# Performance work log

Hardware: AMD Instinct MI355X
Metric: run time of the kernel (lower is better)

Reference implementation:

```python
import jax, jax.numpy as jnp
import numpy as np

N = 65536       # n_nodes
E = 1048576     # n_edges (avg degree 16)
IDX = 256       # index_size
DIN = 512       # gcn_input_size
DH = 512        # gcn_hidden_size
DOUT = 128      # gcn_output_size
S = 256         # sample_size


def gcn_conv(h, W, b, src, dst, n):
    # PyG GCNConv: linear, add self-loops, symmetric deg^-1/2 normalization, scatter-add.
    h = h @ W
    loop = jnp.arange(n)
    s = jnp.concatenate([src, loop])
    d = jnp.concatenate([dst, loop])
    deg = jax.ops.segment_sum(jnp.ones(s.shape[0], h.dtype), d, num_segments=n)
    inv_sqrt = jax.lax.rsqrt(deg)  # deg >= 1 due to self-loops
    norm = inv_sqrt[s] * inv_sqrt[d]
    out = jax.ops.segment_sum(h[s] * norm[:, None], d, num_segments=n)
    return out + b


def _lin_init(k, fan_in, shape):
    bound = 1.0 / np.sqrt(fan_in)
    return jax.random.uniform(k, shape, jnp.float32, -bound, bound)


def setup_inputs() -> dict:
    key = jax.random.key(0)
    ks = jax.random.split(key, 14)
    x = jax.random.normal(ks[0], (N, IDX + 768), jnp.float32)
    edge_index = jax.random.randint(ks[1], (2, E), 0, N, dtype=jnp.int64)
    return {
        "x": x,
        "W_t1": _lin_init(ks[2], IDX, (IDX, DIN)),
        "b_t1": _lin_init(ks[3], IDX, (DIN,)),
        "W_t2": _lin_init(ks[4], 768, (768, DIN)),
        "b_t2": _lin_init(ks[5], 768, (DIN,)),
        "W1": _lin_init(ks[6], DIN, (DIN, DH)),
        "b1": _lin_init(ks[7], DIN, (DH,)),
        "W2": _lin_init(ks[8], DH, (DH, DOUT)),
        "b2": _lin_init(ks[9], DH, (DOUT,)),
        "matrix": jax.random.normal(ks[10], (DOUT, DOUT), jnp.float32),
        "lin_w": _lin_init(ks[11], 1, (2,)),   # nn.Linear(1, 2) weight, squeezed
        "lin_b": _lin_init(ks[12], 1, (2,)),
        "edge_index": edge_index,
    }


def reference(x, W_t1, b_t1, W_t2, b_t2, W1, b1, W2, b2, matrix, lin_w, lin_b, edge_index):
    src, dst = edge_index[0], edge_index[1]
    # dual-input linear fusion
    h = x[:, :IDX] @ W_t1 + b_t1 + x[:, IDX:] @ W_t2 + b_t2
    h = gcn_conv(h, W1, b1, src, dst, N)
    h = jax.nn.relu(h)  # dropout is identity in eval mode
    h = gcn_conv(h, W2, b2, src, dst, N)
    # per-sample bilinear score, batched over chunks
    e = h.reshape(N // S, S, DOUT)
    scores = jnp.einsum('bid,de,bje->bij', e, matrix, e)  # [B, S, S]
    out = scores[..., None] * lin_w + lin_b               # Linear(1, 2)
    return out.reshape(-1, 2)
```

## Files before the change

### kernel.cpp

```cpp
#include <hip/hip_runtime.h>
#include <stdint.h>

#define NN 65536

typedef __attribute__((ext_vector_type(8))) short bf16x8;
typedef __attribute__((ext_vector_type(4))) float f32x4;

__device__ __forceinline__ unsigned short f2bf(float f) {
    unsigned u = __float_as_uint(f);
    u += 0x7fffu + ((u >> 16) & 1u);
    return (unsigned short)(u >> 16);
}
__device__ __forceinline__ float bf2f(unsigned short h) { return __uint_as_float(((unsigned)h) << 16); }
__device__ __forceinline__ float blo(unsigned u) { return __uint_as_float(u << 16); }
__device__ __forceinline__ float bhi(unsigned u) { return __uint_as_float(u & 0xffff0000u); }
__device__ __forceinline__ unsigned pack2(float a, float b) {
    return ((unsigned)f2bf(b) << 16) | (unsigned)f2bf(a);
}

__device__ __forceinline__ void gl_lds16(const void* g, void* l) {
    __builtin_amdgcn_global_load_lds((const __attribute__((address_space(1))) void*)g,
                                     (__attribute__((address_space(3))) void*)l, 16, 0, 0);
}

__global__ void prep_pack(const float* Wt1, const float* Wt2, const float* W1,
                          const float* W2, const float* Mtx,
                          unsigned short* Wcat, unsigned short* W1T,
                          unsigned short* W2T, unsigned short* MTh, unsigned short* MTl) {
    int i = blockIdx.x * 256 + threadIdx.x;
    if (i < 524288) {
        int k = i >> 9, j = i & 511;
        float v = (k < 256) ? Wt1[k * 512 + j] : Wt2[(k - 256) * 512 + j];
        Wcat[i] = f2bf(v);
    } else if (i < 786432) {
        int t = i - 524288; int n = t >> 9, j = t & 511;
        W1T[t] = f2bf(W1[j * 512 + n]);
    } else if (i < 851968) {
        int t = i - 786432; int n = t >> 9, j = t & 511;
        W2T[t] = f2bf(W2[j * 128 + n]);
    } else if (i < 868352) {
        int t = i - 851968; int d = t >> 7, e = t & 127;
        float m = Mtx[e * 128 + d];
        unsigned short h = f2bf(m);
        MTh[t] = h; MTl[t] = f2bf(m - bf2f(h));
    }
}

__global__ void cbias_k(const float* bt1, const float* bt2, const float* W1, float* c) {
    int n = blockIdx.x * 256 + threadIdx.x;
    float acc = 0.f;
    for (int j = 0; j < 512; j++) acc += (bt1[j] + bt2[j]) * W1[j * 512 + n];
    c[n] = acc;
}

__global__ void count_k(const int* dst, int* cnt, int E) {
    int e = blockIdx.x * 256 + threadIdx.x;
    if (e < E) atomicAdd(&cnt[dst[e]], 1);
}
__global__ void red_k(const int* cnt, int* bsum) {
    __shared__ int sm[256];
    int tid = threadIdx.x;
    sm[tid] = cnt[blockIdx.x * 256 + tid];
    __syncthreads();
    for (int s = 128; s > 0; s >>= 1) {
        if (tid < s) sm[tid] += sm[tid + s];
        __syncthreads();
    }
    if (tid == 0) bsum[blockIdx.x] = sm[0];
}
__global__ void scanb_k(const int* bsum, int* boff) {
    __shared__ int sm[256];
    int tid = threadIdx.x;
    int v0 = bsum[tid];
    sm[tid] = v0;
    __syncthreads();
    for (int s = 1; s < 256; s <<= 1) {
        int t = sm[tid];
        if (tid >= s) t += sm[tid - s];
        __syncthreads();
        sm[tid] = t;
        __syncthreads();
    }
    boff[tid] = sm[tid] - v0;
}
__global__ void scanf_k(const int* cnt, const int* boff, int* rowptr, int* cursor, float* invs) {
    __shared__ int sm[256];
    int tid = threadIdx.x;
    int i = blockIdx.x * 256 + tid;
    int v = cnt[i];
    sm[tid] = v;
    __syncthreads();
    for (int s = 1; s < 256; s <<= 1) {
        int t = sm[tid];
        if (tid >= s) t += sm[tid - s];
        __syncthreads();
        sm[tid] = t;
        __syncthreads();
    }
    int incl = sm[tid];
    int base = boff[blockIdx.x];
    int excl = base + incl - v;
    rowptr[i] = excl;
    cursor[i] = excl;
    invs[i] = rsqrtf((float)(v + 1));
    if (i == NN - 1) rowptr[NN] = base + incl;
}
__global__ void fill_k(const int* src, const int* dst, int* cursor, int* colv, int E) {
    int e = blockIdx.x * 256 + threadIdx.x;
    if (e < E) {
        int d = dst[e];
        int p = atomicAdd(&cursor[d], 1);
        colv[p] = src[e];
    }
}

__global__ __launch_bounds__(256, 2) void gemm_bt(const unsigned short* A, const unsigned short* BT,
                                                  unsigned short* C, const float* bias,
                                                  int M, int N, int K) {
    __shared__ __align__(16) unsigned short sA[128 * 32];
    __shared__ __align__(16) unsigned short sB[128 * 32];
    int tid = threadIdx.x, wave = tid >> 6, lane = tid & 63;
    int bm = blockIdx.y * 128, bn = blockIdx.x * 128;
    int wm = (wave >> 1) * 64, wn = (wave & 1) * 64;
    f32x4 acc[4][4];
#pragma unroll
    for (int i = 0; i < 4; i++)
#pragma unroll
        for (int j = 0; j < 4; j++) acc[i][j] = (f32x4){0.f, 0.f, 0.f, 0.f};
    int sr = wave * 32 + (lane >> 2);
    int sc = (lane & 3) * 8;
    const int fr = lane & 15;
    const int fk = (lane >> 4) * 8;
    for (int k0 = 0; k0 < K; k0 += 32) {
        const unsigned short* ga = A + (size_t)(bm + sr) * K + k0 + sc;
        gl_lds16(ga, &sA[sr * 32 + sc]);
        gl_lds16(ga + (size_t)16 * K, &sA[(sr + 16) * 32 + sc]);
        const unsigned short* gb = BT + (size_t)(bn + sr) * K + k0 + sc;
        gl_lds16(gb, &sB[sr * 32 + sc]);
        gl_lds16(gb + (size_t)16 * K, &sB[(sr + 16) * 32 + sc]);
        __syncthreads();
        bf16x8 af[4], bfr[4];
#pragma unroll
        for (int i = 0; i < 4; i++) af[i] = *(const bf16x8*)&sA[(wm + i * 16 + fr) * 32 + fk];
#pragma unroll
        for (int j = 0; j < 4; j++) bfr[j] = *(const bf16x8*)&sB[(wn + j * 16 + fr) * 32 + fk];
#pragma unroll
        for (int i = 0; i < 4; i++)
#pragma unroll
            for (int j = 0; j < 4; j++)
                acc[i][j] = __builtin_amdgcn_mfma_f32_16x16x32_bf16(af[i], bfr[j], acc[i][j], 0, 0, 0);
        __syncthreads();
    }
    int rq = (lane >> 4) * 4;
#pragma unroll
    for (int i = 0; i < 4; i++)
#pragma unroll
        for (int j = 0; j < 4; j++) {
            int col = bn + wn + j * 16 + fr;
            float bb = bias ? bias[col] : 0.f;
#pragma unroll
            for (int r = 0; r < 4; r++) {
                int row = bm + wm + i * 16 + rq + r;
                C[(size_t)row * N + col] = f2bf(acc[i][j][r] + bb);
            }
        }
}

__global__ __launch_bounds__(256, 2) void gemm_f32a(const float* A, const unsigned short* BT,
                                                    unsigned short* C, const float* bias,
                                                    int M, int N, int K) {
    __shared__ __align__(16) unsigned short sA[128 * 32];
    __shared__ __align__(16) unsigned short sB[128 * 32];
    int tid = threadIdx.x, wave = tid >> 6, lane = tid & 63;
    int bm = blockIdx.y * 128, bn = blockIdx.x * 128;
    int wm = (wave >> 1) * 64, wn = (wave & 1) * 64;
    f32x4 acc[4][4];
#pragma unroll
    for (int i = 0; i < 4; i++)
#pragma unroll
        for (int j = 0; j < 4; j++) acc[i][j] = (f32x4){0.f, 0.f, 0.f, 0.f};
    int sr = wave * 32 + (lane >> 2);
    int sc = (lane & 3) * 8;
    const int fr = lane & 15;
    const int fk = (lane >> 4) * 8;
    for (int k0 = 0; k0 < K; k0 += 32) {
#pragma unroll
        for (int i = 0; i < 4; i++) {
            int idx = tid + 256 * i;
            int row = idx >> 3, cg = idx & 7;
            float4 v = *(const float4*)&A[(size_t)(bm + row) * K + k0 + cg * 4];
            ushort4 pk;
            pk.x = f2bf(v.x); pk.y = f2bf(v.y); pk.z = f2bf(v.z); pk.w = f2bf(v.w);
            *(ushort4*)&sA[row * 32 + cg * 4] = pk;
        }
        const unsigned short* gb = BT + (size_t)(bn + sr) * K + k0 + sc;
        gl_lds16(gb, &sB[sr * 32 + sc]);
        gl_lds16(gb + (size_t)16 * K, &sB[(sr + 16) * 32 + sc]);
        __syncthreads();
        bf16x8 af[4], bfr[4];
#pragma unroll
        for (int i = 0; i < 4; i++) af[i] = *(const bf16x8*)&sA[(wm + i * 16 + fr) * 32 + fk];
#pragma unroll
        for (int j = 0; j < 4; j++) bfr[j] = *(const bf16x8*)&sB[(wn + j * 16 + fr) * 32 + fk];
#pragma unroll
        for (int i = 0; i < 4; i++)
#pragma unroll
            for (int j = 0; j < 4; j++)
                acc[i][j] = __builtin_amdgcn_mfma_f32_16x16x32_bf16(af[i], bfr[j], acc[i][j], 0, 0, 0);
        __syncthreads();
    }
    int rq = (lane >> 4) * 4;
#pragma unroll
    for (int i = 0; i < 4; i++)
#pragma unroll
        for (int j = 0; j < 4; j++) {
            int col = bn + wn + j * 16 + fr;
            float bb = bias ? bias[col] : 0.f;
#pragma unroll
            for (int r = 0; r < 4; r++) {
                int row = bm + wm + i * 16 + rq + r;
                C[(size_t)row * N + col] = f2bf(acc[i][j][r] + bb);
            }
        }
}

__global__ __launch_bounds__(256, 2) void gemm_T(const unsigned short* h2h, const unsigned short* h2l,
                                                 const unsigned short* MTh, const unsigned short* MTl,
                                                 unsigned short* Th, unsigned short* Tl) {
    __shared__ __align__(16) unsigned short sA[128 * 32];
    __shared__ __align__(16) unsigned short sB[128 * 32];
    int tid = threadIdx.x, wave = tid >> 6, lane = tid & 63;
    int bm = blockIdx.x * 128;
    int wm = (wave >> 1) * 64, wn = (wave & 1) * 64;
    f32x4 acc[4][4];
#pragma unroll
    for (int i = 0; i < 4; i++)
#pragma unroll
        for (int j = 0; j < 4; j++) acc[i][j] = (f32x4){0.f, 0.f, 0.f, 0.f};
    int sr = wave * 32 + (lane >> 2);
    int sc = (lane & 3) * 8;
    const int fr = lane & 15;
    const int fk = (lane >> 4) * 8;
    const unsigned short* APs[3] = {h2h, h2h, h2l};
    const unsigned short* BPs[3] = {MTh, MTl, MTh};
    for (int it = 0; it < 12; it++) {
        int ph = it >> 2, k0 = (it & 3) * 32;
        const unsigned short* ga = APs[ph] + (size_t)(bm + sr) * 128 + k0 + sc;
        gl_lds16(ga, &sA[sr * 32 + sc]);
        gl_lds16(ga + 16 * 128, &sA[(sr + 16) * 32 + sc]);
        const unsigned short* gb = BPs[ph] + (size_t)sr * 128 + k0 + sc;
        gl_lds16(gb, &sB[sr * 32 + sc]);
        gl_lds16(gb + 16 * 128, &sB[(sr + 16) * 32 + sc]);
        __syncthreads();
        bf16x8 af[4], bfr[4];
#pragma unroll
        for (int i = 0; i < 4; i++) af[i] = *(const bf16x8*)&sA[(wm + i * 16 + fr) * 32 + fk];
#pragma unroll
        for (int j = 0; j < 4; j++) bfr[j] = *(const bf16x8*)&sB[(wn + j * 16 + fr) * 32 + fk];
#pragma unroll
        for (int i = 0; i < 4; i++)
#pragma unroll
            for (int j = 0; j < 4; j++)
                acc[i][j] = __builtin_amdgcn_mfma_f32_16x16x32_bf16(af[i], bfr[j], acc[i][j], 0, 0, 0);
        __syncthreads();
    }
    int rq = (lane >> 4) * 4;
#pragma unroll
    for (int i = 0; i < 4; i++)
#pragma unroll
        for (int j = 0; j < 4; j++) {
            int col = wn + j * 16 + fr;
#pragma unroll
            for (int r = 0; r < 4; r++) {
                int row = bm + wm + i * 16 + rq + r;
                float v = acc[i][j][r];
                unsigned short h = f2bf(v);
                Th[(size_t)row * 128 + col] = h;
                Tl[(size_t)row * 128 + col] = f2bf(v - bf2f(h));
            }
        }
}

__global__ __launch_bounds__(256) void agg512(const unsigned short* t, const int* rowptr,
                                              const int* colv, const float* invs,
                                              const float* bias, unsigned short* outp) {
    int wave = threadIdx.x >> 6, lane = threadIdx.x & 63;
    int node = blockIdx.x * 4 + wave;
    int d0 = lane * 8;
    float acc[8] = {0.f, 0.f, 0.f, 0.f, 0.f, 0.f, 0.f, 0.f};
    int r0 = rowptr[node], r1 = rowptr[node + 1];
    for (int e = r0; e < r1; e++) {
        int s = colv[e];
        float ws = invs[s];
        uint4 v = *(const uint4*)&t[(size_t)s * 512 + d0];
        acc[0] += ws * blo(v.x); acc[1] += ws * bhi(v.x);
        acc[2] += ws * blo(v.y); acc[3] += ws * bhi(v.y);
        acc[4] += ws * blo(v.z); acc[5] += ws * bhi(v.z);
        acc[6] += ws * blo(v.w); acc[7] += ws * bhi(v.w);
    }
    float wd = invs[node], wdd = wd * wd;
    uint4 sv = *(const uint4*)&t[(size_t)node * 512 + d0];
    float sf[8] = {blo(sv.x), bhi(sv.x), blo(sv.y), bhi(sv.y), blo(sv.z), bhi(sv.z), blo(sv.w), bhi(sv.w)};
    float o[8];
#pragma unroll
    for (int k = 0; k < 8; k++) {
        float v = acc[k] * wd + sf[k] * wdd + bias[d0 + k];
        o[k] = v > 0.f ? v : 0.f;
    }
    uint4 pv;
    pv.x = pack2(o[0], o[1]); pv.y = pack2(o[2], o[3]);
    pv.z = pack2(o[4], o[5]); pv.w = pack2(o[6], o[7]);
    *(uint4*)&outp[(size_t)node * 512 + d0] = pv;
}

__global__ __launch_bounds__(256) void agg128(const unsigned short* u, const int* rowptr,
                                              const int* colv, const float* invs,
                                              const float* bias, unsigned short* h2h, unsigned short* h2l) {
    int wave = threadIdx.x >> 6, lane = threadIdx.x & 63;
    int node = blockIdx.x * 4 + wave;
    int q = lane >> 4, ql = lane & 15;
    int d0 = ql * 8;
    float acc[8] = {0.f, 0.f, 0.f, 0.f, 0.f, 0.f, 0.f, 0.f};
    int r0 = rowptr[node], r1 = rowptr[node + 1];
    for (int e = r0 + q; e < r1; e += 4) {
        int s = colv[e];
        float ws = invs[s];
        uint4 v = *(const uint4*)&u[(size_t)s * 128 + d0];
        acc[0] += ws * blo(v.x); acc[1] += ws * bhi(v.x);
        acc[2] += ws * blo(v.y); acc[3] += ws * bhi(v.y);
        acc[4] += ws * blo(v.z); acc[5] += ws * bhi(v.z);
        acc[6] += ws * blo(v.w); acc[7] += ws * bhi(v.w);
    }
#pragma unroll
    for (int k = 0; k < 8; k++) {
        acc[k] += __shfl_xor(acc[k], 16);
        acc[k] += __shfl_xor(acc[k], 32);
    }
    float wd = invs[node], wdd = wd * wd;
    uint4 sv = *(const uint4*)&u[(size_t)node * 128 + d0];
    float sf[8] = {blo(sv.x), bhi(sv.x), blo(sv.y), bhi(sv.y), blo(sv.z), bhi(sv.z), blo(sv.w), bhi(sv.w)};
    unsigned short hh[8], hl[8];
#pragma unroll
    for (int k = 0; k < 8; k++) {
        float v = acc[k] * wd + sf[k] * wdd + bias[d0 + k];
        hh[k] = f2bf(v);
        hl[k] = f2bf(v - bf2f(hh[k]));
    }
    if (q == 0) {
        uint4 ph, pl;
        ph.x = ((unsigned)hh[1] << 16) | hh[0]; ph.y = ((unsigned)hh[3] << 16) | hh[2];
        ph.z = ((unsigned)hh[5] << 16) | hh[4]; ph.w = ((unsigned)hh[7] << 16) | hh[6];
        pl.x = ((unsigned)hl[1] << 16) | hl[0]; pl.y = ((unsigned)hl[3] << 16) | hl[2];
        pl.z = ((unsigned)hl[5] << 16) | hl[4]; pl.w = ((unsigned)hl[7] << 16) | hl[6];
        *(uint4*)&h2h[(size_t)node * 128 + d0] = ph;
        *(uint4*)&h2l[(size_t)node * 128 + d0] = pl;
    }
}

__global__ __launch_bounds__(256, 2) void bilinear_k(const unsigned short* Th, const unsigned short* Tl,
                                                     const unsigned short* Eh, const float* lin_w,
                                                     const float* lin_b, float* outp) {
    int tid = threadIdx.x, wave = tid >> 6, lane = tid & 63;
    int b = blockIdx.x >> 1, half = blockIdx.x & 1;
    int fr = lane & 15, q = lane >> 4;
    int irow0 = b * 256 + half * 128 + wave * 32;
    bf16x8 Ah[2][4], Al[2][4];
#pragma unroll
    for (int it = 0; it < 2; it++)
#pragma unroll
        for (int kk = 0; kk < 4; kk++) {
            size_t off = (size_t)(irow0 + it * 16 + fr) * 128 + kk * 32 + q * 8;
            Ah[it][kk] = *(const bf16x8*)&Th[off];
            Al[it][kk] = *(const bf16x8*)&Tl[off];
        }
    float w0 = lin_w[0], w1 = lin_w[1], c0 = lin_b[0], c1 = lin_b[1];
    for (int jt = 0; jt < 16; jt++) {
        bf16x8 Bf[4];
#pragma unroll
        for (int kk = 0; kk < 4; kk++)
            Bf[kk] = *(const bf16x8*)&Eh[(size_t)(b * 256 + jt * 16 + fr) * 128 + kk * 32 + q * 8];
#pragma unroll
        for (int it = 0; it < 2; it++) {
            f32x4 acc = (f32x4){0.f, 0.f, 0.f, 0.f};
#pragma unroll
            for (int kk = 0; kk < 4; kk++) {
                acc = __builtin_amdgcn_mfma_f32_16x16x32_bf16(Ah[it][kk], Bf[kk], acc, 0, 0, 0);
                acc = __builtin_amdgcn_mfma_f32_16x16x32_bf16(Al[it][kk], Bf[kk], acc, 0, 0, 0);
            }
#pragma unroll
            for (int r = 0; r < 4; r++) {
                int iloc = half * 128 + wave * 32 + it * 16 + q * 4 + r;
                int jloc = jt * 16 + fr;
                size_t o = ((size_t)b * 65536 + (size_t)iloc * 256 + jloc) * 2;
                float s = acc[r];
                float2 ov;
                ov.x = fmaf(s, w0, c0);
                ov.y = fmaf(s, w1, c1);
                *(float2*)&outp[o] = ov;
            }
        }
    }
}

extern "C" void kernel_launch(void* const* d_in, const int* in_sizes, int n_in,
                              void* d_out, int out_size, void* d_ws, size_t ws_size,
                              hipStream_t stream) {
    const float* x   = (const float*)d_in[0];
    const float* Wt1 = (const float*)d_in[1];
    const float* bt1 = (const float*)d_in[2];
    const float* Wt2 = (const float*)d_in[3];
    const float* bt2 = (const float*)d_in[4];
    const float* W1  = (const float*)d_in[5];
    const float* b1  = (const float*)d_in[6];
    const float* W2  = (const float*)d_in[7];
    const float* b2  = (const float*)d_in[8];
    const float* Mtx = (const float*)d_in[9];
    const float* lw  = (const float*)d_in[10];
    const float* lb  = (const float*)d_in[11];
    const int*   ei  = (const int*)d_in[12];
    int E = in_sizes[12] / 2;
    const int* srcp = ei;
    const int* dstp = ei + E;

    unsigned char* p = (unsigned char*)d_ws;
    size_t off = 0;
    auto alloc = [&](size_t bytes) -> void* {
        void* r = p + off;
        off = (off + bytes + 255) & ~(size_t)255;
        return r;
    };
    int*   cnt    = (int*)alloc((size_t)NN * 4);
    int*   rowptr = (int*)alloc(((size_t)NN + 1) * 4);
    int*   cursor = (int*)alloc((size_t)NN * 4);
    float* invs   = (float*)alloc((size_t)NN * 4);
    int*   bsum   = (int*)alloc(256 * 4);
    int*   boff   = (int*)alloc(256 * 4);
    int*   colv   = (int*)alloc((size_t)E * 4);
    unsigned short* Wcat   = (unsigned short*)alloc(524288 * 2);
    unsigned short* W1T    = (unsigned short*)alloc(262144 * 2);
    unsigned short* W2T    = (unsigned short*)alloc(65536 * 2);
    unsigned short* MTh    = (unsigned short*)alloc(16384 * 2);
    unsigned short* MTl    = (unsigned short*)alloc(16384 * 2);
    float*          cbias  = (float*)alloc(512 * 4);
    unsigned short* WcombT = (unsigned short*)alloc(524288 * 2);
    unsigned short* t1     = (unsigned short*)alloc((size_t)NN * 512 * 2);
    unsigned short* h1     = (unsigned short*)alloc((size_t)NN * 512 * 2);
    unsigned short* uu     = (unsigned short*)alloc((size_t)NN * 128 * 2);
    unsigned short* Th  = t1;
    unsigned short* Tl  = t1 + (size_t)NN * 128;
    unsigned short* h2h = h1;
    unsigned short* h2l = h1 + (size_t)NN * 128;

    hipMemsetAsync(cnt, 0, (size_t)NN * 4, stream);
    prep_pack<<<3392, 256, 0, stream>>>(Wt1, Wt2, W1, W2, Mtx, Wcat, W1T, W2T, MTh, MTl);
    cbias_k<<<2, 256, 0, stream>>>(bt1, bt2, W1, cbias);
    count_k<<<(E + 255) / 256, 256, 0, stream>>>(dstp, cnt, E);
    red_k<<<256, 256, 0, stream>>>(cnt, bsum);
    scanb_k<<<1, 256, 0, stream>>>(bsum, boff);
    scanf_k<<<256, 256, 0, stream>>>(cnt, boff, rowptr, cursor, invs);
    fill_k<<<(E + 255) / 256, 256, 0, stream>>>(srcp, dstp, cursor, colv, E);
    gemm_bt<<<dim3(8, 4), 256, 0, stream>>>(W1T, Wcat, WcombT, nullptr, 512, 1024, 512);
    gemm_f32a<<<dim3(4, 512), 256, 0, stream>>>(x, WcombT, t1, cbias, NN, 512, 1024);
    agg512<<<NN / 4, 256, 0, stream>>>(t1, rowptr, colv, invs, b1, h1);
    gemm_bt<<<dim3(1, 512), 256, 0, stream>>>(h1, W2T, uu, nullptr, NN, 128, 512);
    agg128<<<NN / 4, 256, 0, stream>>>(uu, rowptr, colv, invs, b2, h2h, h2l);
    gemm_T<<<512, 256, 0, stream>>>(h2h, h2l, MTh, MTl, Th, Tl);
    bilinear_k<<<512, 256, 0, stream>>>(Th, Tl, h2h, lw, lb, (float*)d_out);
}
```

Baseline: 952.2 us.

## Double-buffer f32 GEMM, remap blocks by XCD, unroll aggregation, split bias reduction

```diff
diff --git a/kernel.cpp b/kernel.cpp
--- a/kernel.cpp
+++ b/kernel.cpp
@@ -47,10 +47,21 @@
 }
 
 __global__ void cbias_k(const float* bt1, const float* bt2, const float* W1, float* c) {
-    int n = blockIdx.x * 256 + threadIdx.x;
+    __shared__ float sm[256];
+    int t = threadIdx.x;
+    int n = blockIdx.x * 32 + (t & 31);
+    int jp = t >> 5;
     float acc = 0.f;
-    for (int j = 0; j < 512; j++) acc += (bt1[j] + bt2[j]) * W1[j * 512 + n];
-    c[n] = acc;
+    for (int j = jp * 64; j < jp * 64 + 64; j++)
+        acc += (bt1[j] + bt2[j]) * W1[j * 512 + n];
+    sm[t] = acc;
+    __syncthreads();
+    if (t < 32) {
+        float a = 0.f;
+#pragma unroll
+        for (int p = 0; p < 8; p++) a += sm[p * 32 + t];
+        c[blockIdx.x * 32 + t] = a;
+    }
 }
 
 __global__ void count_k(const int* dst, int* cnt, int E) {
@@ -167,12 +178,14 @@
 }
 
 __global__ __launch_bounds__(256, 2) void gemm_f32a(const float* A, const unsigned short* BT,
-                                                    unsigned short* C, const float* bias,
-                                                    int M, int N, int K) {
-    __shared__ __align__(16) unsigned short sA[128 * 32];
-    __shared__ __align__(16) unsigned short sB[128 * 32];
+                                                    unsigned short* C, const float* bias) {
+    const int K = 1024, N = 512;
+    __shared__ __align__(16) unsigned short sA[2][128 * 32];
+    __shared__ __align__(16) unsigned short sB[2][128 * 32];
     int tid = threadIdx.x, wave = tid >> 6, lane = tid & 63;
-    int bm = blockIdx.y * 128, bn = blockIdx.x * 128;
+    int b = blockIdx.x;
+    int xcd = b & 7, jn = (b >> 3) & 3, tt = b >> 5;
+    int bm = (tt * 8 + xcd) * 128, bn = jn * 128;
     int wm = (wave >> 1) * 64, wn = (wave & 1) * 64;
     f32x4 acc[4][4];
 #pragma unroll
@@ -183,25 +196,44 @@
     int sc = (lane & 3) * 8;
     const int fr = lane & 15;
     const int fk = (lane >> 4) * 8;
-    for (int k0 = 0; k0 < K; k0 += 32) {
+    int ar = tid >> 3, ac = (tid & 7) * 4;
+    const float* Abase = A + (size_t)(bm + ar) * K + ac;
+    const unsigned short* Bbase = BT + (size_t)(bn + sr) * K + sc;
+    float4 ra[4];
+    auto loadA = [&](int k0) {
+#pragma unroll
+        for (int i = 0; i < 4; i++)
+            ra[i] = *(const float4*)(Abase + (size_t)(32 * i) * K + k0);
+    };
+    auto stageA = [&](int buf) {
 #pragma unroll
         for (int i = 0; i < 4; i++) {
-            int idx = tid + 256 * i;
-            int row = idx >> 3, cg = idx & 7;
-            float4 v = *(const float4*)&A[(size_t)(bm + row) * K + k0 + cg * 4];
             ushort4 pk;
-            pk.x = f2bf(v.x); pk.y = f2bf(v.y); pk.z = f2bf(v.z); pk.w = f2bf(v.w);
-            *(ushort4*)&sA[row * 32 + cg * 4] = pk;
-        }
-        const unsigned short* gb = BT + (size_t)(bn + sr) * K + k0 + sc;
-        gl_lds16(gb, &sB[sr * 32 + sc]);
-        gl_lds16(gb + (size_t)16 * K, &sB[(sr + 16) * 32 + sc]);
-        __syncthreads();
+            pk.x = f2bf(ra[i].x); pk.y = f2bf(ra[i].y); pk.z = f2bf(ra[i].z); pk.w = f2bf(ra[i].w);
+            *(ushort4*)&sA[buf][(ar + 32 * i) * 32 + ac] = pk;
+        }
+    };
+    auto stageB = [&](int buf, int k0) {
+        gl_lds16(Bbase + k0, &sB[buf][sr * 32 + sc]);
+        gl_lds16(Bbase + (size_t)16 * K + k0, &sB[buf][(sr + 16) * 32 + sc]);
+    };
+    loadA(0);
+    stageB(0, 0);
+    stageA(0);
+    loadA(32);
+    __syncthreads();
+    for (int k = 0; k < 32; k++) {
+        int cur = k & 1, nxt = cur ^ 1;
+        if (k < 31) {
+            stageB(nxt, (k + 1) * 32);
+            stageA(nxt);
+        }
+        if (k < 30) loadA((k + 2) * 32);
         bf16x8 af[4], bfr[4];
 #pragma unroll
-        for (int i = 0; i < 4; i++) af[i] = *(const bf16x8*)&sA[(wm + i * 16 + fr) * 32 + fk];
-#pragma unroll
-        for (int j = 0; j < 4; j++) bfr[j] = *(const bf16x8*)&sB[(wn + j * 16 + fr) * 32 + fk];
+        for (int i = 0; i < 4; i++) af[i] = *(const bf16x8*)&sA[cur][(wm + i * 16 + fr) * 32 + fk];
+#pragma unroll
+        for (int j = 0; j < 4; j++) bfr[j] = *(const bf16x8*)&sB[cur][(wn + j * 16 + fr) * 32 + fk];
 #pragma unroll
         for (int i = 0; i < 4; i++)
 #pragma unroll
@@ -215,7 +247,7 @@
 #pragma unroll
         for (int j = 0; j < 4; j++) {
             int col = bn + wn + j * 16 + fr;
-            float bb = bias ? bias[col] : 0.f;
+            float bb = bias[col];
 #pragma unroll
             for (int r = 0; r < 4; r++) {
                 int row = bm + wm + i * 16 + rq + r;
@@ -289,7 +321,22 @@
     int d0 = lane * 8;
     float acc[8] = {0.f, 0.f, 0.f, 0.f, 0.f, 0.f, 0.f, 0.f};
     int r0 = rowptr[node], r1 = rowptr[node + 1];
-    for (int e = r0; e < r1; e++) {
+    int e = r0;
+    for (; e + 2 <= r1; e += 2) {
+        int s0 = colv[e], s1 = colv[e + 1];
+        float w0 = invs[s0], w1 = invs[s1];
+        uint4 v0 = *(const uint4*)&t[(size_t)s0 * 512 + d0];
+        uint4 v1 = *(const uint4*)&t[(size_t)s1 * 512 + d0];
+        acc[0] += w0 * blo(v0.x) + w1 * blo(v1.x);
+        acc[1] += w0 * bhi(v0.x) + w1 * bhi(v1.x);
+        acc[2] += w0 * blo(v0.y) + w1 * blo(v1.y);
+        acc[3] += w0 * bhi(v0.y) + w1 * bhi(v1.y);
+        acc[4] += w0 * blo(v0.z) + w1 * blo(v1.z);
+        acc[5] += w0 * bhi(v0.z) + w1 * bhi(v1.z);
+        acc[6] += w0 * blo(v0.w) + w1 * blo(v1.w);
+        acc[7] += w0 * bhi(v0.w) + w1 * bhi(v1.w);
+    }
+    if (e < r1) {
         int s = colv[e];
         float ws = invs[s];
         uint4 v = *(const uint4*)&t[(size_t)s * 512 + d0];
@@ -453,14 +500,14 @@
 
     hipMemsetAsync(cnt, 0, (size_t)NN * 4, stream);
     prep_pack<<<3392, 256, 0, stream>>>(Wt1, Wt2, W1, W2, Mtx, Wcat, W1T, W2T, MTh, MTl);
-    cbias_k<<<2, 256, 0, stream>>>(bt1, bt2, W1, cbias);
+    cbias_k<<<16, 256, 0, stream>>>(bt1, bt2, W1, cbias);
     count_k<<<(E + 255) / 256, 256, 0, stream>>>(dstp, cnt, E);
     red_k<<<256, 256, 0, stream>>>(cnt, bsum);
     scanb_k<<<1, 256, 0, stream>>>(bsum, boff);
     scanf_k<<<256, 256, 0, stream>>>(cnt, boff, rowptr, cursor, invs);
     fill_k<<<(E + 255) / 256, 256, 0, stream>>>(srcp, dstp, cursor, colv, E);
     gemm_bt<<<dim3(8, 4), 256, 0, stream>>>(W1T, Wcat, WcombT, nullptr, 512, 1024, 512);
-    gemm_f32a<<<dim3(4, 512), 256, 0, stream>>>(x, WcombT, t1, cbias, NN, 512, 1024);
+    gemm_f32a<<<2048, 256, 0, stream>>>(x, WcombT, t1, cbias);
     agg512<<<NN / 4, 256, 0, stream>>>(t1, rowptr, colv, invs, b1, h1);
     gemm_bt<<<dim3(1, 512), 256, 0, stream>>>(h1, W2T, uu, nullptr, NN, 128, 512);
     agg128<<<NN / 4, 256, 0, stream>>>(uu, rowptr, colv, invs, b2, h2h, h2l);
```

Result: no change. 938.5 us (-1.4%).
